# Optimization experiments

Hardware: AMD Instinct MI355X
Metric: run time of the kernel (lower is better)

Reference implementation:

```python
import jax, jax.numpy as jnp
import numpy as np

D_PAIR, C, N_HEAD = 128, 32, 4
HC = N_HEAD * C

def setup_inputs() -> dict:
    key = jax.random.key(0)
    ks = jax.random.split(key, 8)
    B, N = 1, 384
    Z_raw = jax.random.normal(ks[0], (B, N, N, D_PAIR), dtype=jnp.float32)
    Z_mask = jnp.ones((B, N, N), dtype=jnp.float32)
    s = 1.0 / np.sqrt(D_PAIR)
    return {
        'Z_raw': Z_raw,
        'Z_mask': Z_mask,
        'ln_w': jnp.ones((D_PAIR,), jnp.float32),
        'ln_b': jnp.zeros((D_PAIR,), jnp.float32),
        'W_b': jax.random.uniform(ks[1], (D_PAIR, N_HEAD), jnp.float32, -s, s),
        'W_qkv': jax.random.uniform(ks[2], (D_PAIR, 3 * HC), jnp.float32, -s, s),
        'W_gate': jnp.zeros((D_PAIR, HC), jnp.float32),
        'gating_bias': jnp.ones((HC,), jnp.float32),
        'W_o': jnp.zeros((HC, D_PAIR), jnp.float32),
        'out_bias': jnp.zeros((D_PAIR,), jnp.float32),
    }

def reference(Z_raw, Z_mask, ln_w, ln_b, W_b, W_qkv, W_gate, gating_bias, W_o, out_bias):
    B, N, _, D = Z_raw.shape
    # LayerNorm over d_pair
    mu = jnp.mean(Z_raw, axis=-1, keepdims=True)
    var = jnp.var(Z_raw, axis=-1, keepdims=True)
    Z = (Z_raw - mu) * jax.lax.rsqrt(var + 1e-5) * ln_w + ln_b
    # nonbatched triangle bias: [B, h, q, k]
    bias = jnp.einsum('bqkh->bhqk', jnp.einsum('bqkd,dh->bqkh', Z, W_b))
    # qkv projection: [B, N(rows), N, 3*h*c]
    qkv = jnp.einsum('bind,de->bine', Z, W_qkv)
    q, k, v = jnp.split(qkv, 3, axis=-1)
    resh = lambda t: t.reshape(B, N, N, N_HEAD, C).transpose(0, 1, 3, 2, 4)  # [B,i,h,n,c]
    q, k, v = resh(q) * (C ** -0.5), resh(k), resh(v)
    logits = jnp.einsum('bihqc,bihkc->bihqk', q, k)
    mask_bias = (Z_mask - 1.0) * 1e9  # [B, i, k]
    logits = logits + mask_bias[:, :, None, None, :] + bias[:, None, :, :, :]
    weights = jax.nn.softmax(logits, axis=-1)
    wa = jnp.einsum('bihqk,bihkc->bihqc', weights, v)
    wa = wa.transpose(0, 1, 3, 2, 4).reshape(B, N, N, HC)
    gate = jax.nn.sigmoid(jnp.einsum('bind,de->bine', Z, W_gate) + gating_bias)
    out = jnp.einsum('bine,ed->bind', gate * wa, W_o)
    # bias_dropout_add with training=False -> plain bias + residual add
    return Z_raw + out + out_bias
```

## Files before the change

### kernel.cpp

```cpp
#include <hip/hip_runtime.h>
#include <hip/hip_bf16.h>

#define NN 384
#define DP 128
#define NHEAD 4
#define CH 32
#define HCC 128

typedef __hip_bfloat16 bf16;
typedef __bf16 bf16x8 __attribute__((ext_vector_type(8)));
typedef __bf16 bf16x4 __attribute__((ext_vector_type(4)));
typedef float floatx4 __attribute__((ext_vector_type(4)));

#define QKSTRIDE 40
#define VPSTRIDE 408
#define WSTRIDE 136

__device__ __forceinline__ float b2f(bf16 x){ return __bfloat162float(x); }
__device__ __forceinline__ bf16 f2b(float x){ return __float2bfloat16(x); }

__global__ __launch_bounds__(256) void wt_kernel(
    const float* __restrict__ Wqkv, __bf16* __restrict__ Wt)
{
  int idx = blockIdx.x * 256 + threadIdx.x;
  int d = idx / NN, col = idx - d * NN;
  Wt[col * DP + d] = (__bf16)Wqkv[idx];
}

__global__ __launch_bounds__(256) void wgo_kernel(
    const float* __restrict__ Wg, const float* __restrict__ Wo,
    __bf16* __restrict__ WgT, __bf16* __restrict__ WoT)
{
  int idx = blockIdx.x * 256 + threadIdx.x;
  int r = idx >> 7, c = idx & 127;
  WgT[idx] = (__bf16)Wg[c * 128 + r];
  WoT[idx] = (__bf16)Wo[c * 128 + r];
}

__global__ __launch_bounds__(256) void ln_bias_kernel(
    const float* __restrict__ Zr, const float* __restrict__ lnw,
    const float* __restrict__ lnb, const float* __restrict__ Wb,
    bf16* __restrict__ Zn, float* __restrict__ bias)
{
  int t = threadIdx.x;
  int grp = t >> 5, lane32 = t & 31;
  int pos = blockIdx.x * 8 + grp;
  size_t base = (size_t)pos * DP;
  const float4 x = *(const float4*)(Zr + base + lane32 * 4);
  float s  = x.x + x.y + x.z + x.w;
  float s2 = x.x*x.x + x.y*x.y + x.z*x.z + x.w*x.w;
  #pragma unroll
  for (int m = 1; m < 32; m <<= 1){ s += __shfl_xor(s, m); s2 += __shfl_xor(s2, m); }
  float mean = s * (1.0f / DP);
  float var  = s2 * (1.0f / DP) - mean * mean;
  float rstd = rsqrtf(var + 1e-5f);
  const float4 w4 = *(const float4*)(lnw + lane32 * 4);
  const float4 b4 = *(const float4*)(lnb + lane32 * 4);
  float z0 = (x.x - mean) * rstd * w4.x + b4.x;
  float z1 = (x.y - mean) * rstd * w4.y + b4.y;
  float z2 = (x.z - mean) * rstd * w4.z + b4.z;
  float z3 = (x.w - mean) * rstd * w4.w + b4.w;
  bf16x4 zb = { (__bf16)z0, (__bf16)z1, (__bf16)z2, (__bf16)z3 };
  *(bf16x4*)((__bf16*)Zn + base + lane32 * 4) = zb;
  const float4 wb0 = *(const float4*)(Wb + (lane32 * 4 + 0) * NHEAD);
  const float4 wb1 = *(const float4*)(Wb + (lane32 * 4 + 1) * NHEAD);
  const float4 wb2 = *(const float4*)(Wb + (lane32 * 4 + 2) * NHEAD);
  const float4 wb3 = *(const float4*)(Wb + (lane32 * 4 + 3) * NHEAD);
  float p0 = z0*wb0.x + z1*wb1.x + z2*wb2.x + z3*wb3.x;
  float p1 = z0*wb0.y + z1*wb1.y + z2*wb2.y + z3*wb3.y;
  float p2 = z0*wb0.z + z1*wb1.z + z2*wb2.z + z3*wb3.z;
  float p3 = z0*wb0.w + z1*wb1.w + z2*wb2.w + z3*wb3.w;
  #pragma unroll
  for (int m = 1; m < 32; m <<= 1){
    p0 += __shfl_xor(p0, m); p1 += __shfl_xor(p1, m);
    p2 += __shfl_xor(p2, m); p3 += __shfl_xor(p3, m);
  }
  if (lane32 == 0){
    bias[0 * NN * NN + pos] = p0;
    bias[1 * NN * NN + pos] = p1;
    bias[2 * NN * NN + pos] = p2;
    bias[3 * NN * NN + pos] = p3;
  }
}

__global__ __launch_bounds__(256, 1) void attn_kernel(
    const __bf16* __restrict__ Zn, const __bf16* __restrict__ Wt,
    const float* __restrict__ Zm, const float* __restrict__ bias,
    __bf16* __restrict__ wa)
{
  __shared__ __align__(16) __bf16 qs[NN * QKSTRIDE];
  __shared__ __align__(16) __bf16 ks[NN * QKSTRIDE];
  __shared__ __align__(16) __bf16 vs[CH * VPSTRIDE];
  __shared__ __align__(16) __bf16 ps[4 * 16 * VPSTRIDE];
  __shared__ float maskb[NN];

  int i = blockIdx.x >> 2;
  int h = blockIdx.x & 3;
  int t = threadIdx.x;
  int wv = t >> 6;
  int lane = t & 63;
  int m16 = lane & 15;
  int quad = lane >> 4;

  for (int k = t; k < NN; k += 256)
    maskb[k] = (Zm[(size_t)i * NN + k] - 1.0f) * 1e9f;

  const float qscale = 0.17677669529663687f;

  for (int mt = wv * 6; mt < wv * 6 + 6; mt++){
    bf16x8 afr[4];
    const __bf16* arow = Zn + (size_t)(i * NN + mt * 16 + m16) * DP + quad * 8;
    #pragma unroll
    for (int kc = 0; kc < 4; kc++) afr[kc] = *(const bf16x8*)(arow + kc * 32);
    for (int nt = 0; nt < 6; nt++){
      int mat = nt >> 1;
      int colbase = mat * HCC + h * CH + (nt & 1) * 16;
      const __bf16* brow = Wt + (size_t)(colbase + m16) * DP + quad * 8;
      floatx4 acc = {0.f, 0.f, 0.f, 0.f};
      #pragma unroll
      for (int kc = 0; kc < 4; kc++){
        bf16x8 bfr = *(const bf16x8*)(brow + kc * 32);
        acc = __builtin_amdgcn_mfma_f32_16x16x32_bf16(afr[kc], bfr, acc, 0, 0, 0);
      }
      int ccol = (nt & 1) * 16 + m16;
      #pragma unroll
      for (int reg = 0; reg < 4; reg++){
        int row = mt * 16 + quad * 4 + reg;
        float v = acc[reg];
        if (mat == 0)      qs[row * QKSTRIDE + ccol] = (__bf16)(v * qscale);
        else if (mat == 1) ks[row * QKSTRIDE + ccol] = (__bf16)v;
        else               vs[ccol * VPSTRIDE + row] = (__bf16)v;
      }
    }
  }
  __syncthreads();

  const float* brow_base = bias + (size_t)h * NN * NN;
  __bf16* pw = ps + wv * 16 * VPSTRIDE;

  for (int s = 0; s < 6; s++){
    int strip = wv * 6 + s;
    bf16x8 qf = *(const bf16x8*)(qs + (strip * 16 + m16) * QKSTRIDE + quad * 8);
    floatx4 sacc[24];
    #pragma unroll
    for (int kt = 0; kt < 24; kt++){
      bf16x8 kf = *(const bf16x8*)(ks + (kt * 16 + m16) * QKSTRIDE + quad * 8);
      floatx4 z = {0.f, 0.f, 0.f, 0.f};
      sacc[kt] = __builtin_amdgcn_mfma_f32_16x16x32_bf16(qf, kf, z, 0, 0, 0);
    }
    float mx[4] = {-1e30f, -1e30f, -1e30f, -1e30f};
    #pragma unroll
    for (int kt = 0; kt < 24; kt++){
      int col = kt * 16 + m16;
      float mb = maskb[col];
      #pragma unroll
      for (int reg = 0; reg < 4; reg++){
        int row = strip * 16 + quad * 4 + reg;
        float v = sacc[kt][reg] + brow_base[(size_t)row * NN + col] + mb;
        sacc[kt][reg] = v;
        mx[reg] = fmaxf(mx[reg], v);
      }
    }
    #pragma unroll
    for (int reg = 0; reg < 4; reg++)
      for (int msk = 1; msk < 16; msk <<= 1)
        mx[reg] = fmaxf(mx[reg], __shfl_xor(mx[reg], msk));
    float sm[4] = {0.f, 0.f, 0.f, 0.f};
    #pragma unroll
    for (int kt = 0; kt < 24; kt++){
      int col = kt * 16 + m16;
      #pragma unroll
      for (int reg = 0; reg < 4; reg++){
        float p = __expf(sacc[kt][reg] - mx[reg]);
        sm[reg] += p;
        pw[(quad * 4 + reg) * VPSTRIDE + col] = (__bf16)p;
      }
    }
    #pragma unroll
    for (int reg = 0; reg < 4; reg++)
      for (int msk = 1; msk < 16; msk <<= 1)
        sm[reg] += __shfl_xor(sm[reg], msk);
    float inv[4];
    #pragma unroll
    for (int reg = 0; reg < 4; reg++) inv[reg] = 1.0f / sm[reg];

    floatx4 oacc[2] = {{0.f,0.f,0.f,0.f},{0.f,0.f,0.f,0.f}};
    #pragma unroll
    for (int kc = 0; kc < 12; kc++){
      bf16x8 pa = *(const bf16x8*)(pw + m16 * VPSTRIDE + kc * 32 + quad * 8);
      #pragma unroll
      for (int ct = 0; ct < 2; ct++){
        bf16x8 vb = *(const bf16x8*)(vs + (ct * 16 + m16) * VPSTRIDE + kc * 32 + quad * 8);
        oacc[ct] = __builtin_amdgcn_mfma_f32_16x16x32_bf16(pa, vb, oacc[ct], 0, 0, 0);
      }
    }
    #pragma unroll
    for (int ct = 0; ct < 2; ct++){
      #pragma unroll
      for (int reg = 0; reg < 4; reg++){
        int row = strip * 16 + quad * 4 + reg;
        wa[(size_t)(i * NN + row) * HCC + h * CH + ct * 16 + m16] =
            (__bf16)(oacc[ct][reg] * inv[reg]);
      }
    }
  }
}

__global__ __launch_bounds__(256, 1) void out_kernel(
    const float* __restrict__ Zr, const __bf16* __restrict__ Zn,
    const __bf16* __restrict__ wa, const __bf16* __restrict__ WgT,
    const float* __restrict__ gb, const __bf16* __restrict__ WoT,
    const float* __restrict__ ob, float* __restrict__ out)
{
  __shared__ __align__(16) __bf16 wgs[128 * WSTRIDE];
  __shared__ __align__(16) __bf16 wos[128 * WSTRIDE];
  __shared__ __align__(16) __bf16 gsh[4][16 * WSTRIDE];
  __shared__ float gbs[HCC], obs[DP];

  int t = threadIdx.x;
  int wv = t >> 6, lane = t & 63;
  int m16 = lane & 15, quad = lane >> 4;

  for (int idx = t * 8; idx < 128 * 128; idx += 256 * 8){
    int r = idx >> 7, c = idx & 127;
    *(bf16x8*)(wgs + r * WSTRIDE + c) = *(const bf16x8*)(WgT + idx);
    *(bf16x8*)(wos + r * WSTRIDE + c) = *(const bf16x8*)(WoT + idx);
  }
  if (t < 128){ gbs[t] = gb[t]; obs[t] = ob[t]; }
  __syncthreads();

  int mbase = blockIdx.x * 128;
  __bf16* gstrip = gsh[wv];

  for (int sp = 0; sp < 2; sp++){
    int row0 = mbase + (sp * 4 + wv) * 16;
    bf16x8 afr[4];
    const __bf16* arow = Zn + (size_t)(row0 + m16) * DP + quad * 8;
    #pragma unroll
    for (int kc = 0; kc < 4; kc++) afr[kc] = *(const bf16x8*)(arow + kc * 32);
    #pragma unroll
    for (int nt = 0; nt < 8; nt++){
      floatx4 acc = {0.f, 0.f, 0.f, 0.f};
      #pragma unroll
      for (int kc = 0; kc < 4; kc++){
        bf16x8 bfr = *(const bf16x8*)(wgs + (nt * 16 + m16) * WSTRIDE + kc * 32 + quad * 8);
        acc = __builtin_amdgcn_mfma_f32_16x16x32_bf16(afr[kc], bfr, acc, 0, 0, 0);
      }
      int col = nt * 16 + m16;
      #pragma unroll
      for (int reg = 0; reg < 4; reg++){
        int row = row0 + quad * 4 + reg;
        float g = 1.0f / (1.0f + __expf(-(acc[reg] + gbs[col])));
        float w = __bfloat162float(wa[(size_t)row * HCC + col]);
        gstrip[(quad * 4 + reg) * WSTRIDE + col] = (__bf16)(g * w);
      }
    }
    bf16x8 gfr[4];
    #pragma unroll
    for (int kc = 0; kc < 4; kc++)
      gfr[kc] = *(const bf16x8*)(gstrip + m16 * WSTRIDE + kc * 32 + quad * 8);
    #pragma unroll
    for (int nt = 0; nt < 8; nt++){
      floatx4 acc = {0.f, 0.f, 0.f, 0.f};
      #pragma unroll
      for (int kc = 0; kc < 4; kc++){
        bf16x8 bfr = *(const bf16x8*)(wos + (nt * 16 + m16) * WSTRIDE + kc * 32 + quad * 8);
        acc = __builtin_amdgcn_mfma_f32_16x16x32_bf16(gfr[kc], bfr, acc, 0, 0, 0);
      }
      int col = nt * 16 + m16;
      #pragma unroll
      for (int reg = 0; reg < 4; reg++){
        int row = row0 + quad * 4 + reg;
        size_t off = (size_t)row * DP + col;
        out[off] = Zr[off] + acc[reg] + obs[col];
      }
    }
  }
}

extern "C" void kernel_launch(void* const* d_in, const int* in_sizes, int n_in,
                              void* d_out, int out_size, void* d_ws, size_t ws_size,
                              hipStream_t stream)
{
  const float* Zr   = (const float*)d_in[0];
  const float* Zm   = (const float*)d_in[1];
  const float* lnw  = (const float*)d_in[2];
  const float* lnb  = (const float*)d_in[3];
  const float* Wb   = (const float*)d_in[4];
  const float* Wqkv = (const float*)d_in[5];
  const float* Wg   = (const float*)d_in[6];
  const float* gb   = (const float*)d_in[7];
  const float* Wo   = (const float*)d_in[8];
  const float* ob   = (const float*)d_in[9];
  float* out = (float*)d_out;

  char* ws = (char*)d_ws;
  size_t off = 0;
  bf16*   Zn   = (bf16*)(ws + off);           off += (size_t)NN * NN * DP * 2;
  float*  bias = (float*)(ws + off);          off += (size_t)NHEAD * NN * NN * 4;
  bf16*   wa   = (bf16*)(ws + off);           off += (size_t)NN * NN * HCC * 2;
  __bf16* Wt   = (__bf16*)(ws + off);         off += (size_t)3 * HCC * DP * 2;
  __bf16* WgT  = (__bf16*)(ws + off);         off += (size_t)DP * HCC * 2;
  __bf16* WoT  = (__bf16*)(ws + off);         off += (size_t)HCC * DP * 2;

  wt_kernel<<<(3 * HCC * DP) / 256, 256, 0, stream>>>(Wqkv, Wt);
  wgo_kernel<<<(DP * HCC) / 256, 256, 0, stream>>>(Wg, Wo, WgT, WoT);
  ln_bias_kernel<<<NN * NN / 8, 256, 0, stream>>>(Zr, lnw, lnb, Wb, Zn, bias);
  attn_kernel<<<NN * NHEAD, 256, 0, stream>>>((const __bf16*)Zn, Wt, Zm, bias, (__bf16*)wa);
  out_kernel<<<NN * NN / 128, 256, 0, stream>>>(Zr, (const __bf16*)Zn, (const __bf16*)wa,
                                                WgT, gb, WoT, ob, out);
}
```

Before: 496.3 us.

## Shrink attention LDS with XOR swizzle, chunk softmax into PV, raise occupancy

The attention kernel replaces its padded Q/K/V/P shared-memory buffers with unpadded XOR-swizzled layouts. It interleaves the exp/softmax with the P·V MFMAs using a small per-wave 16x32 P chunk, so the full probability strip is no longer staged. Together these cut LDS use enough to allow two blocks per CU (launch_bounds 256,2), and the QK MFMA loop gets a raised wave priority. The output kernel fuses the gate and output projections per 32-column k-chunk with a smaller gate buffer and also targets two blocks per CU. The risk is that register pressure under the tighter bound causes spills, and the extra LDS syncs within each wave add latency.

After: 690.9 us. 1.39x slower.

```diff
diff --git a/kernel.cpp b/kernel.cpp
--- a/kernel.cpp
+++ b/kernel.cpp
@@ -12,9 +12,8 @@
 typedef __bf16 bf16x4 __attribute__((ext_vector_type(4)));
 typedef float floatx4 __attribute__((ext_vector_type(4)));
 
-#define QKSTRIDE 40
-#define VPSTRIDE 408
 #define WSTRIDE 136
+#define GSTRIDE 40
 
 __device__ __forceinline__ float b2f(bf16 x){ return __bfloat162float(x); }
 __device__ __forceinline__ bf16 f2b(float x){ return __float2bfloat16(x); }
@@ -83,15 +82,15 @@
   }
 }
 
-__global__ __launch_bounds__(256, 1) void attn_kernel(
+__global__ __launch_bounds__(256, 2) void attn_kernel(
     const __bf16* __restrict__ Zn, const __bf16* __restrict__ Wt,
     const float* __restrict__ Zm, const float* __restrict__ bias,
     __bf16* __restrict__ wa)
 {
-  __shared__ __align__(16) __bf16 qs[NN * QKSTRIDE];
-  __shared__ __align__(16) __bf16 ks[NN * QKSTRIDE];
-  __shared__ __align__(16) __bf16 vs[CH * VPSTRIDE];
-  __shared__ __align__(16) __bf16 ps[4 * 16 * VPSTRIDE];
+  __shared__ __align__(128) __bf16 qs[NN * 32];
+  __shared__ __align__(128) __bf16 ks[NN * 32];
+  __shared__ __align__(128) __bf16 vs[CH * NN];
+  __shared__ __align__(128) __bf16 pch[4 * 16 * 32];
   __shared__ float maskb[NN];
 
   int i = blockIdx.x >> 2;
@@ -112,6 +111,7 @@
     const __bf16* arow = Zn + (size_t)(i * NN + mt * 16 + m16) * DP + quad * 8;
     #pragma unroll
     for (int kc = 0; kc < 4; kc++) afr[kc] = *(const bf16x8*)(arow + kc * 32);
+    #pragma unroll
     for (int nt = 0; nt < 6; nt++){
       int mat = nt >> 1;
       int colbase = mat * HCC + h * CH + (nt & 1) * 16;
@@ -127,27 +127,31 @@
       for (int reg = 0; reg < 4; reg++){
         int row = mt * 16 + quad * 4 + reg;
         float v = acc[reg];
-        if (mat == 0)      qs[row * QKSTRIDE + ccol] = (__bf16)(v * qscale);
-        else if (mat == 1) ks[row * QKSTRIDE + ccol] = (__bf16)v;
-        else               vs[ccol * VPSTRIDE + row] = (__bf16)v;
+        if (mat == 0)      qs[(row * 32 + ccol) ^ ((row & 7) << 3)] = (__bf16)(v * qscale);
+        else if (mat == 1) ks[(row * 32 + ccol) ^ ((row & 7) << 3)] = (__bf16)v;
+        else               vs[(ccol * NN + row) ^ ((ccol & 7) << 3)] = (__bf16)v;
       }
     }
   }
   __syncthreads();
 
   const float* brow_base = bias + (size_t)h * NN * NN;
-  __bf16* pw = ps + wv * 16 * VPSTRIDE;
+  __bf16* pw = pch + wv * 512;
 
   for (int s = 0; s < 6; s++){
     int strip = wv * 6 + s;
-    bf16x8 qf = *(const bf16x8*)(qs + (strip * 16 + m16) * QKSTRIDE + quad * 8);
+    int qrow = strip * 16 + m16;
+    bf16x8 qf = *(const bf16x8*)(qs + ((qrow * 32 + quad * 8) ^ ((qrow & 7) << 3)));
     floatx4 sacc[24];
+    __builtin_amdgcn_s_setprio(1);
     #pragma unroll
     for (int kt = 0; kt < 24; kt++){
-      bf16x8 kf = *(const bf16x8*)(ks + (kt * 16 + m16) * QKSTRIDE + quad * 8);
+      int krow = kt * 16 + m16;
+      bf16x8 kf = *(const bf16x8*)(ks + ((krow * 32 + quad * 8) ^ ((krow & 7) << 3)));
       floatx4 z = {0.f, 0.f, 0.f, 0.f};
       sacc[kt] = __builtin_amdgcn_mfma_f32_16x16x32_bf16(qf, kf, z, 0, 0, 0);
     }
+    __builtin_amdgcn_s_setprio(0);
     float mx[4] = {-1e30f, -1e30f, -1e30f, -1e30f};
     #pragma unroll
     for (int kt = 0; kt < 24; kt++){
@@ -163,37 +167,41 @@
     }
     #pragma unroll
     for (int reg = 0; reg < 4; reg++)
+      #pragma unroll
       for (int msk = 1; msk < 16; msk <<= 1)
         mx[reg] = fmaxf(mx[reg], __shfl_xor(mx[reg], msk));
+
     float sm[4] = {0.f, 0.f, 0.f, 0.f};
-    #pragma unroll
-    for (int kt = 0; kt < 24; kt++){
-      int col = kt * 16 + m16;
-      #pragma unroll
-      for (int reg = 0; reg < 4; reg++){
-        float p = __expf(sacc[kt][reg] - mx[reg]);
-        sm[reg] += p;
-        pw[(quad * 4 + reg) * VPSTRIDE + col] = (__bf16)p;
+    floatx4 oacc[2] = {{0.f,0.f,0.f,0.f},{0.f,0.f,0.f,0.f}};
+    #pragma unroll
+    for (int kc = 0; kc < 12; kc++){
+      #pragma unroll
+      for (int ktl = 0; ktl < 2; ktl++){
+        int kt = kc * 2 + ktl;
+        #pragma unroll
+        for (int reg = 0; reg < 4; reg++){
+          float p = __expf(sacc[kt][reg] - mx[reg]);
+          sm[reg] += p;
+          int r = quad * 4 + reg;
+          pw[(r * 32 + ktl * 16 + m16) ^ ((r & 7) << 3)] = (__bf16)p;
+        }
+      }
+      bf16x8 pa = *(const bf16x8*)(pw + ((m16 * 32 + quad * 8) ^ ((m16 & 7) << 3)));
+      #pragma unroll
+      for (int ct = 0; ct < 2; ct++){
+        int c = ct * 16 + m16;
+        bf16x8 vb = *(const bf16x8*)(vs + ((c * NN + kc * 32 + quad * 8) ^ ((c & 7) << 3)));
+        oacc[ct] = __builtin_amdgcn_mfma_f32_16x16x32_bf16(pa, vb, oacc[ct], 0, 0, 0);
       }
     }
     #pragma unroll
     for (int reg = 0; reg < 4; reg++)
+      #pragma unroll
       for (int msk = 1; msk < 16; msk <<= 1)
         sm[reg] += __shfl_xor(sm[reg], msk);
     float inv[4];
     #pragma unroll
     for (int reg = 0; reg < 4; reg++) inv[reg] = 1.0f / sm[reg];
-
-    floatx4 oacc[2] = {{0.f,0.f,0.f,0.f},{0.f,0.f,0.f,0.f}};
-    #pragma unroll
-    for (int kc = 0; kc < 12; kc++){
-      bf16x8 pa = *(const bf16x8*)(pw + m16 * VPSTRIDE + kc * 32 + quad * 8);
-      #pragma unroll
-      for (int ct = 0; ct < 2; ct++){
-        bf16x8 vb = *(const bf16x8*)(vs + (ct * 16 + m16) * VPSTRIDE + kc * 32 + quad * 8);
-        oacc[ct] = __builtin_amdgcn_mfma_f32_16x16x32_bf16(pa, vb, oacc[ct], 0, 0, 0);
-      }
-    }
     #pragma unroll
     for (int ct = 0; ct < 2; ct++){
       #pragma unroll
@@ -206,15 +214,15 @@
   }
 }
 
-__global__ __launch_bounds__(256, 1) void out_kernel(
+__global__ __launch_bounds__(256, 2) void out_kernel(
     const float* __restrict__ Zr, const __bf16* __restrict__ Zn,
     const __bf16* __restrict__ wa, const __bf16* __restrict__ WgT,
     const float* __restrict__ gb, const __bf16* __restrict__ WoT,
     const float* __restrict__ ob, float* __restrict__ out)
 {
-  __shared__ __align__(16) __bf16 wgs[128 * WSTRIDE];
-  __shared__ __align__(16) __bf16 wos[128 * WSTRIDE];
-  __shared__ __align__(16) __bf16 gsh[4][16 * WSTRIDE];
+  __shared__ __align__(128) __bf16 wgs[128 * WSTRIDE];
+  __shared__ __align__(128) __bf16 wos[128 * WSTRIDE];
+  __shared__ __align__(128) __bf16 gsh[4][16 * GSTRIDE];
   __shared__ float gbs[HCC], obs[DP];
 
   int t = threadIdx.x;
@@ -238,41 +246,46 @@
     const __bf16* arow = Zn + (size_t)(row0 + m16) * DP + quad * 8;
     #pragma unroll
     for (int kc = 0; kc < 4; kc++) afr[kc] = *(const bf16x8*)(arow + kc * 32);
+
+    floatx4 acc[8];
+    #pragma unroll
+    for (int nt = 0; nt < 8; nt++) acc[nt] = (floatx4){0.f, 0.f, 0.f, 0.f};
+
+    #pragma unroll
+    for (int kcg = 0; kcg < 4; kcg++){
+      #pragma unroll
+      for (int ntg = 0; ntg < 2; ntg++){
+        int col16 = kcg * 32 + ntg * 16;
+        floatx4 ga = {0.f, 0.f, 0.f, 0.f};
+        #pragma unroll
+        for (int kc = 0; kc < 4; kc++){
+          bf16x8 bfr = *(const bf16x8*)(wgs + (col16 + m16) * WSTRIDE + kc * 32 + quad * 8);
+          ga = __builtin_amdgcn_mfma_f32_16x16x32_bf16(afr[kc], bfr, ga, 0, 0, 0);
+        }
+        int col = col16 + m16;
+        #pragma unroll
+        for (int reg = 0; reg < 4; reg++){
+          int row = row0 + quad * 4 + reg;
+          float g = 1.0f / (1.0f + __expf(-(ga[reg] + gbs[col])));
+          float w = b2f(wa[(size_t)row * HCC + col]);
+          gstrip[(quad * 4 + reg) * GSTRIDE + ntg * 16 + m16] = f2b(g * w);
+        }
+      }
+      bf16x8 gfr = *(const bf16x8*)(gstrip + m16 * GSTRIDE + quad * 8);
+      #pragma unroll
+      for (int nt = 0; nt < 8; nt++){
+        bf16x8 bfr = *(const bf16x8*)(wos + (nt * 16 + m16) * WSTRIDE + kcg * 32 + quad * 8);
+        acc[nt] = __builtin_amdgcn_mfma_f32_16x16x32_bf16(gfr, bfr, acc[nt], 0, 0, 0);
+      }
+    }
     #pragma unroll
     for (int nt = 0; nt < 8; nt++){
-      floatx4 acc = {0.f, 0.f, 0.f, 0.f};
-      #pragma unroll
-      for (int kc = 0; kc < 4; kc++){
-        bf16x8 bfr = *(const bf16x8*)(wgs + (nt * 16 + m16) * WSTRIDE + kc * 32 + quad * 8);
-        acc = __builtin_amdgcn_mfma_f32_16x16x32_bf16(afr[kc], bfr, acc, 0, 0, 0);
-      }
-      int col = nt * 16 + m16;
-      #pragma unroll
-      for (int reg = 0; reg < 4; reg++){
-        int row = row0 + quad * 4 + reg;
-        float g = 1.0f / (1.0f + __expf(-(acc[reg] + gbs[col])));
-        float w = __bfloat162float(wa[(size_t)row * HCC + col]);
-        gstrip[(quad * 4 + reg) * WSTRIDE + col] = (__bf16)(g * w);
-      }
-    }
-    bf16x8 gfr[4];
-    #pragma unroll
-    for (int kc = 0; kc < 4; kc++)
-      gfr[kc] = *(const bf16x8*)(gstrip + m16 * WSTRIDE + kc * 32 + quad * 8);
-    #pragma unroll
-    for (int nt = 0; nt < 8; nt++){
-      floatx4 acc = {0.f, 0.f, 0.f, 0.f};
-      #pragma unroll
-      for (int kc = 0; kc < 4; kc++){
-        bf16x8 bfr = *(const bf16x8*)(wos + (nt * 16 + m16) * WSTRIDE + kc * 32 + quad * 8);
-        acc = __builtin_amdgcn_mfma_f32_16x16x32_bf16(gfr[kc], bfr, acc, 0, 0, 0);
-      }
       int col = nt * 16 + m16;
       #pragma unroll
       for (int reg = 0; reg < 4; reg++){
         int row = row0 + quad * 4 + reg;
         size_t off = (size_t)row * DP + col;
-        out[off] = Zr[off] + acc[reg] + obs[col];
+        out[off] = Zr[off] + acc[nt][reg] + obs[col];
       }
     }
   }
```

## Keep softmax probabilities in registers and swizzle attention LDS layout

Applied to the files above, without the earlier changes.

The attention kernel now computes S^T (K as the A operand) so that each lane holds a query row's scores in the exact layout needed as the A operand of the P·V MFMA. This removes the per-wave P buffer in shared memory. The change also replaces padded strides with XOR-swizzled unpadded Q/K/V tiles, loads the pair bias as contiguous float4 rows, and reduces max/sum with two shuffles instead of sixteen. With the smaller LDS footprint, launch bounds allow two blocks per CU, and block indices are remapped across XCDs. Normalization is applied before the bf16 cast of P, at the cost of more register pressure.

Measured after the change: 800.0 us. 61.2% more time.

```diff
diff --git a/kernel.cpp b/kernel.cpp
--- a/kernel.cpp
+++ b/kernel.cpp
@@ -12,8 +12,6 @@
 typedef __bf16 bf16x4 __attribute__((ext_vector_type(4)));
 typedef float floatx4 __attribute__((ext_vector_type(4)));
 
-#define QKSTRIDE 40
-#define VPSTRIDE 408
 #define WSTRIDE 136
 
 __device__ __forceinline__ float b2f(bf16 x){ return __bfloat162float(x); }
@@ -83,19 +81,20 @@
   }
 }
 
-__global__ __launch_bounds__(256, 1) void attn_kernel(
+__global__ __launch_bounds__(256, 2) void attn_kernel(
     const __bf16* __restrict__ Zn, const __bf16* __restrict__ Wt,
     const float* __restrict__ Zm, const float* __restrict__ bias,
     __bf16* __restrict__ wa)
 {
-  __shared__ __align__(16) __bf16 qs[NN * QKSTRIDE];
-  __shared__ __align__(16) __bf16 ks[NN * QKSTRIDE];
-  __shared__ __align__(16) __bf16 vs[CH * VPSTRIDE];
-  __shared__ __align__(16) __bf16 ps[4 * 16 * VPSTRIDE];
-  __shared__ float maskb[NN];
-
-  int i = blockIdx.x >> 2;
-  int h = blockIdx.x & 3;
+  __shared__ __align__(128) __bf16 qs[NN * 32];
+  __shared__ __align__(128) __bf16 ks[NN * 32];
+  __shared__ __align__(128) __bf16 vs[CH * NN];
+  __shared__ __align__(16) float maskb[NN];
+
+  int bid = blockIdx.x;
+  int b = (bid & 7) * 192 + (bid >> 3);
+  int i = b >> 2;
+  int h = b & 3;
   int t = threadIdx.x;
   int wv = t >> 6;
   int lane = t & 63;
@@ -112,6 +111,7 @@
     const __bf16* arow = Zn + (size_t)(i * NN + mt * 16 + m16) * DP + quad * 8;
     #pragma unroll
     for (int kc = 0; kc < 4; kc++) afr[kc] = *(const bf16x8*)(arow + kc * 32);
+    #pragma unroll
     for (int nt = 0; nt < 6; nt++){
       int mat = nt >> 1;
       int colbase = mat * HCC + h * CH + (nt & 1) * 16;
@@ -127,80 +127,100 @@
       for (int reg = 0; reg < 4; reg++){
         int row = mt * 16 + quad * 4 + reg;
         float v = acc[reg];
-        if (mat == 0)      qs[row * QKSTRIDE + ccol] = (__bf16)(v * qscale);
-        else if (mat == 1) ks[row * QKSTRIDE + ccol] = (__bf16)v;
-        else               vs[ccol * VPSTRIDE + row] = (__bf16)v;
+        if (mat == 0)      qs[(row * 32 + ccol) ^ ((row & 7) << 3)] = (__bf16)(v * qscale);
+        else if (mat == 1) ks[(row * 32 + ccol) ^ ((row & 7) << 3)] = (__bf16)v;
+        else               vs[(ccol * NN + row) ^ ((ccol & 7) << 3)] = (__bf16)v;
       }
     }
   }
   __syncthreads();
 
   const float* brow_base = bias + (size_t)h * NN * NN;
-  __bf16* pw = ps + wv * 16 * VPSTRIDE;
 
   for (int s = 0; s < 6; s++){
     int strip = wv * 6 + s;
-    bf16x8 qf = *(const bf16x8*)(qs + (strip * 16 + m16) * QKSTRIDE + quad * 8);
+    int qrow = strip * 16 + m16;
+    bf16x8 qf = *(const bf16x8*)(qs + ((qrow * 32 + quad * 8) ^ ((qrow & 7) << 3)));
+
     floatx4 sacc[24];
+    __builtin_amdgcn_s_setprio(1);
+    #pragma unroll
+    for (int kc = 0; kc < 12; kc++){
+      #pragma unroll
+      for (int tb = 0; tb < 2; tb++){
+        int krow = kc * 32 + ((m16 & 12) << 1) + tb * 4 + (m16 & 3);
+        bf16x8 kf = *(const bf16x8*)(ks + ((krow * 32 + quad * 8) ^ ((krow & 7) << 3)));
+        floatx4 z = {0.f, 0.f, 0.f, 0.f};
+        sacc[kc * 2 + tb] = __builtin_amdgcn_mfma_f32_16x16x32_bf16(kf, qf, z, 0, 0, 0);
+      }
+    }
+    __builtin_amdgcn_s_setprio(0);
+
+    float mx = -1e30f;
+    #pragma unroll
+    for (int kc = 0; kc < 12; kc++){
+      #pragma unroll
+      for (int tb = 0; tb < 2; tb++){
+        int k0 = kc * 32 + quad * 8 + tb * 4;
+        const float4 bb = *(const float4*)(brow_base + (size_t)qrow * NN + k0);
+        const float4 mm = *(const float4*)(maskb + k0);
+        floatx4 v = sacc[kc * 2 + tb];
+        v[0] += bb.x + mm.x;
+        v[1] += bb.y + mm.y;
+        v[2] += bb.z + mm.z;
+        v[3] += bb.w + mm.w;
+        sacc[kc * 2 + tb] = v;
+        mx = fmaxf(mx, fmaxf(fmaxf(v[0], v[1]), fmaxf(v[2], v[3])));
+      }
+    }
+    mx = fmaxf(mx, __shfl_xor(mx, 16));
+    mx = fmaxf(mx, __shfl_xor(mx, 32));
+
+    float sm = 0.f;
     #pragma unroll
     for (int kt = 0; kt < 24; kt++){
-      bf16x8 kf = *(const bf16x8*)(ks + (kt * 16 + m16) * QKSTRIDE + quad * 8);
-      floatx4 z = {0.f, 0.f, 0.f, 0.f};
-      sacc[kt] = __builtin_amdgcn_mfma_f32_16x16x32_bf16(qf, kf, z, 0, 0, 0);
-    }
-    float mx[4] = {-1e30f, -1e30f, -1e30f, -1e30f};
-    #pragma unroll
-    for (int kt = 0; kt < 24; kt++){
-      int col = kt * 16 + m16;
-      float mb = maskb[col];
-      #pragma unroll
-      for (int reg = 0; reg < 4; reg++){
-        int row = strip * 16 + quad * 4 + reg;
-        float v = sacc[kt][reg] + brow_base[(size_t)row * NN + col] + mb;
-        sacc[kt][reg] = v;
-        mx[reg] = fmaxf(mx[reg], v);
-      }
-    }
-    #pragma unroll
-    for (int reg = 0; reg < 4; reg++)
-      for (int msk = 1; msk < 16; msk <<= 1)
-        mx[reg] = fmaxf(mx[reg], __shfl_xor(mx[reg], msk));
-    float sm[4] = {0.f, 0.f, 0.f, 0.f};
-    #pragma unroll
-    for (int kt = 0; kt < 24; kt++){
-      int col = kt * 16 + m16;
-      #pragma unroll
-      for (int reg = 0; reg < 4; reg++){
-        float p = __expf(sacc[kt][reg] - mx[reg]);
-        sm[reg] += p;
-        pw[(quad * 4 + reg) * VPSTRIDE + col] = (__bf16)p;
-      }
-    }
-    #pragma unroll
-    for (int reg = 0; reg < 4; reg++)
-      for (int msk = 1; msk < 16; msk <<= 1)
-        sm[reg] += __shfl_xor(sm[reg], msk);
-    float inv[4];
-    #pragma unroll
-    for (int reg = 0; reg < 4; reg++) inv[reg] = 1.0f / sm[reg];
+      floatx4 v = sacc[kt];
+      #pragma unroll
+      for (int reg = 0; reg < 4; reg++){
+        float p = __expf(v[reg] - mx);
+        sm += p;
+        v[reg] = p;
+      }
+      sacc[kt] = v;
+    }
+    sm += __shfl_xor(sm, 16);
+    sm += __shfl_xor(sm, 32);
+    float inv = 1.0f / sm;
 
     floatx4 oacc[2] = {{0.f,0.f,0.f,0.f},{0.f,0.f,0.f,0.f}};
     #pragma unroll
     for (int kc = 0; kc < 12; kc++){
-      bf16x8 pa = *(const bf16x8*)(pw + m16 * VPSTRIDE + kc * 32 + quad * 8);
+      floatx4 pa0 = sacc[kc * 2];
+      floatx4 pa1 = sacc[kc * 2 + 1];
+      bf16x8 pa;
+      pa[0] = (__bf16)(pa0[0] * inv);
+      pa[1] = (__bf16)(pa0[1] * inv);
+      pa[2] = (__bf16)(pa0[2] * inv);
+      pa[3] = (__bf16)(pa0[3] * inv);
+      pa[4] = (__bf16)(pa1[0] * inv);
+      pa[5] = (__bf16)(pa1[1] * inv);
+      pa[6] = (__bf16)(pa1[2] * inv);
+      pa[7] = (__bf16)(pa1[3] * inv);
       #pragma unroll
       for (int ct = 0; ct < 2; ct++){
-        bf16x8 vb = *(const bf16x8*)(vs + (ct * 16 + m16) * VPSTRIDE + kc * 32 + quad * 8);
+        int c = ct * 16 + m16;
+        bf16x8 vb = *(const bf16x8*)(vs + ((c * NN + kc * 32 + quad * 8) ^ ((c & 7) << 3)));
         oacc[ct] = __builtin_amdgcn_mfma_f32_16x16x32_bf16(pa, vb, oacc[ct], 0, 0, 0);
       }
     }
+
     #pragma unroll
     for (int ct = 0; ct < 2; ct++){
       #pragma unroll
       for (int reg = 0; reg < 4; reg++){
         int row = strip * 16 + quad * 4 + reg;
         wa[(size_t)(i * NN + row) * HCC + h * CH + ct * 16 + m16] =
-            (__bf16)(oacc[ct][reg] * inv[reg]);
+            (__bf16)(oacc[ct][reg]);
       }
     }
   }
@@ -251,8 +271,8 @@
       for (int reg = 0; reg < 4; reg++){
         int row = row0 + quad * 4 + reg;
         float g = 1.0f / (1.0f + __expf(-(acc[reg] + gbs[col])));
-        float w = __bfloat162float(wa[(size_t)row * HCC + col]);
-        gstrip[(quad * 4 + reg) * WSTRIDE + col] = (__bf16)(g * w);
+        float w = b2f(wa[(size_t)row * HCC + col]);
+        gstrip[(quad * 4 + reg) * WSTRIDE + col] = f2b(g * w);
       }
     }
     bf16x8 gfr[4];
```
